# Kernel optimization log

Hardware: AMD Instinct MI355X
Metric: run time of the kernel (lower is better)

The kernel has to match this reference:

```python
import jax, jax.numpy as jnp
import numpy as np

B, N, D = 8, 4096, 2


def setup_inputs() -> dict:
    key = jax.random.key(0)
    k1, k2 = jax.random.split(key)
    y_true = jax.random.normal(k1, (B, N, D), dtype=jnp.float32)
    y_pred = jax.random.normal(k2, (B, N, D), dtype=jnp.float32)
    return {"y_true": y_true, "y_pred": y_pred}


def reference(y_true, y_pred):
    # Bidirectional Chamfer distance (chamferdist semantics):
    # squared-Euclidean NN distances, sum over points, mean over batch, both directions.
    xx = jnp.sum(y_true * y_true, axis=-1)                      # [B, N]
    yy = jnp.sum(y_pred * y_pred, axis=-1)                      # [B, N]
    xy = jnp.einsum('bnd,bmd->bnm', y_true, y_pred)             # [B, N, N]
    d2 = jnp.maximum(xx[:, :, None] + yy[:, None, :] - 2.0 * xy, 0.0)  # [B, N, N]
    cd_fwd = jnp.mean(jnp.sum(jnp.min(d2, axis=2), axis=1))     # true -> pred
    cd_bwd = jnp.mean(jnp.sum(jnp.min(d2, axis=1), axis=1))     # pred -> true
    # EMD approximation: cumsum over the last (coordinate) axis, squared diff, mean.
    emd = jnp.mean(jnp.mean(jnp.square(jnp.cumsum(y_true, axis=-1) - jnp.cumsum(y_pred, axis=-1)), axis=-1))
    return cd_fwd + cd_bwd + emd
```

## Files before the change

### kernel.cpp

```cpp
#include <hip/hip_runtime.h>
#include <math.h>

#define BB    8
#define NN    4096
#define DIRS  2
#define TPB   256
#define Q     16
#define RSIZE 128
#define RC    (NN / RSIZE)
#define CDN   (DIRS * BB * NN)
#define RBLK  128

__global__ __launch_bounds__(TPB) void chamfer_kernel(
    const float* __restrict__ y_true, const float* __restrict__ y_pred,
    float* __restrict__ part)
{
    __shared__ float4 refs[RSIZE];
    const int rc  = blockIdx.x;
    const int dir = blockIdx.y;
    const int b   = blockIdx.z;

    const float2* qbase = (const float2*)(dir == 0 ? y_true : y_pred) + (size_t)b * NN;
    const float2* rbase = (const float2*)(dir == 0 ? y_pred : y_true) + (size_t)b * NN;

    const int t = threadIdx.x;
    if (t < RSIZE) {
        float2 r = rbase[rc * RSIZE + t];
        refs[t] = make_float4(-2.f * r.x, -2.f * r.y,
                              r.x * r.x + r.y * r.y, 0.f);
    }
    __syncthreads();

    float qx[Q], qy[Q], m[Q];
    #pragma unroll
    for (int j = 0; j < Q; ++j) {
        float2 qv = qbase[j * TPB + t];
        qx[j] = qv.x; qy[j] = qv.y; m[j] = INFINITY;
    }

    #pragma unroll 4
    for (int k = 0; k < RSIZE; ++k) {
        float4 r = refs[k];
        #pragma unroll
        for (int j = 0; j < Q; ++j) {
            float d = fmaf(qy[j], r.y, fmaf(qx[j], r.x, r.z));
            m[j] = fminf(m[j], d);
        }
    }

    #pragma unroll
    for (int j = 0; j < Q; ++j) {
        int q = j * TPB + t;
        float v = fmaxf(m[j] + (qx[j] * qx[j] + qy[j] * qy[j]), 0.f);
        part[(size_t)rc * CDN + ((size_t)dir * BB + b) * NN + q] = v;
    }
}

__global__ __launch_bounds__(TPB) void reduce_kernel(
    const float* __restrict__ y_true, const float* __restrict__ y_pred,
    const float* __restrict__ part, float* __restrict__ blocksum)
{
    const float cd_scale  = 1.0f / (float)BB;
    const float emd_scale = 1.0f / (2.0f * (float)BB * (float)NN);

    float acc = 0.f;
    const int gsz = gridDim.x * blockDim.x;
    const int gid = blockIdx.x * blockDim.x + threadIdx.x;

    for (int i = gid; i < CDN; i += gsz) {
        float mv = part[i];
        #pragma unroll
        for (int rc = 1; rc < RC; ++rc)
            mv = fminf(mv, part[(size_t)rc * CDN + i]);
        acc += mv * cd_scale;
    }

    const float2* tp = (const float2*)y_true;
    const float2* pp = (const float2*)y_pred;
    for (int i = gid; i < BB * NN; i += gsz) {
        float2 tv = tp[i], pv = pp[i];
        float c1 = tv.x - pv.x;
        float c2 = (tv.x + tv.y) - (pv.x + pv.y);
        acc = fmaf(c1 * emd_scale, c1, acc);
        acc = fmaf(c2 * emd_scale, c2, acc);
    }

    #pragma unroll
    for (int off = 32; off > 0; off >>= 1)
        acc += __shfl_down(acc, off, 64);

    __shared__ float wsum[TPB / 64];
    const int lane = threadIdx.x & 63, wid = threadIdx.x >> 6;
    if (lane == 0) wsum[wid] = acc;
    __syncthreads();
    if (threadIdx.x == 0) {
        float s = 0.f;
        #pragma unroll
        for (int w = 0; w < TPB / 64; ++w) s += wsum[w];
        blocksum[blockIdx.x] = s;
    }
}

__global__ void final_kernel(const float* __restrict__ blocksum,
                             float* __restrict__ out)
{
    float v = blocksum[threadIdx.x] + blocksum[threadIdx.x + 64];
    #pragma unroll
    for (int off = 32; off > 0; off >>= 1)
        v += __shfl_down(v, off, 64);
    if (threadIdx.x == 0) out[0] = v;
}

extern "C" void kernel_launch(void* const* d_in, const int* in_sizes, int n_in,
                              void* d_out, int out_size, void* d_ws, size_t ws_size,
                              hipStream_t stream) {
    const float* y_true = (const float*)d_in[0];
    const float* y_pred = (const float*)d_in[1];
    float* out = (float*)d_out;

    float* part     = (float*)d_ws;
    float* blocksum = part + (size_t)RC * CDN;

    chamfer_kernel<<<dim3(RC, DIRS, BB), TPB, 0, stream>>>(y_true, y_pred, part);
    reduce_kernel<<<RBLK, TPB, 0, stream>>>(y_true, y_pred, part, blocksum);
    final_kernel<<<1, 64, 0, stream>>>(blocksum, out);
}
```

Measured before the change: 80.93 us.

## Fuse chamfer, reduce and final kernels into one cooperative kernel

Merges the three kernels into a single cooperative launch. A grid-wide sync separates the nearest-neighbour pass from the reduction, and each block then adds its partial sum to the output with an atomicAdd. Block 0 zeroes the output before the grid sync. This removes two kernel launches and the intermediate blocksum buffer, at the cost of a grid barrier, the cooperative-launch requirement that all 512 blocks be co-resident, and a float summation order that is no longer deterministic.

```diff
diff --git a/kernel.cpp b/kernel.cpp
--- a/kernel.cpp
+++ b/kernel.cpp
@@ -1,5 +1,8 @@
 #include <hip/hip_runtime.h>
+#include <hip/hip_cooperative_groups.h>
 #include <math.h>
+
+namespace cg = cooperative_groups;
 
 #define BB    8
 #define NN    4096
@@ -9,26 +12,31 @@
 #define RSIZE 128
 #define RC    (NN / RSIZE)
 #define CDN   (DIRS * BB * NN)
-#define RBLK  128
+#define NBLK  (RC * DIRS * BB)
 
-__global__ __launch_bounds__(TPB) void chamfer_kernel(
+__global__ __launch_bounds__(TPB) void fused_kernel(
     const float* __restrict__ y_true, const float* __restrict__ y_pred,
-    float* __restrict__ part)
+    float* __restrict__ part, float* __restrict__ out)
 {
     __shared__ float4 refs[RSIZE];
-    const int rc  = blockIdx.x;
-    const int dir = blockIdx.y;
-    const int b   = blockIdx.z;
+    __shared__ float wsum[TPB / 64];
+
+    const int bid = blockIdx.x;
+    const int rc  = bid & (RC - 1);
+    const int db  = bid >> 5;
+    const int dir = db >> 3;
+    const int b   = db & (BB - 1);
+    const int t   = threadIdx.x;
 
     const float2* qbase = (const float2*)(dir == 0 ? y_true : y_pred) + (size_t)b * NN;
     const float2* rbase = (const float2*)(dir == 0 ? y_pred : y_true) + (size_t)b * NN;
 
-    const int t = threadIdx.x;
     if (t < RSIZE) {
         float2 r = rbase[rc * RSIZE + t];
         refs[t] = make_float4(-2.f * r.x, -2.f * r.y,
                               r.x * r.x + r.y * r.y, 0.f);
     }
+    if (bid == 0 && t == 0) out[0] = 0.f;
     __syncthreads();
 
     float qx[Q], qy[Q], m[Q];
@@ -52,63 +60,48 @@
     for (int j = 0; j < Q; ++j) {
         int q = j * TPB + t;
         float v = fmaxf(m[j] + (qx[j] * qx[j] + qy[j] * qy[j]), 0.f);
-        part[(size_t)rc * CDN + ((size_t)dir * BB + b) * NN + q] = v;
+        part[(size_t)rc * CDN + (size_t)db * NN + q] = v;
     }
-}
 
-__global__ __launch_bounds__(TPB) void reduce_kernel(
-    const float* __restrict__ y_true, const float* __restrict__ y_pred,
-    const float* __restrict__ part, float* __restrict__ blocksum)
-{
+    cg::this_grid().sync();
+
     const float cd_scale  = 1.0f / (float)BB;
     const float emd_scale = 1.0f / (2.0f * (float)BB * (float)NN);
 
     float acc = 0.f;
-    const int gsz = gridDim.x * blockDim.x;
-    const int gid = blockIdx.x * blockDim.x + threadIdx.x;
 
-    for (int i = gid; i < CDN; i += gsz) {
+    if (t < 128) {
+        int i = bid * 128 + t;
         float mv = part[i];
         #pragma unroll
-        for (int rc = 1; rc < RC; ++rc)
-            mv = fminf(mv, part[(size_t)rc * CDN + i]);
+        for (int r = 1; r < RC; ++r)
+            mv = fminf(mv, part[(size_t)r * CDN + i]);
         acc += mv * cd_scale;
     }
 
-    const float2* tp = (const float2*)y_true;
-    const float2* pp = (const float2*)y_pred;
-    for (int i = gid; i < BB * NN; i += gsz) {
-        float2 tv = tp[i], pv = pp[i];
-        float c1 = tv.x - pv.x;
-        float c2 = (tv.x + tv.y) - (pv.x + pv.y);
-        acc = fmaf(c1 * emd_scale, c1, acc);
-        acc = fmaf(c2 * emd_scale, c2, acc);
+    {
+        int gid = bid * TPB + t;
+        if (gid < BB * NN) {
+            float2 tv = ((const float2*)y_true)[gid];
+            float2 pv = ((const float2*)y_pred)[gid];
+            float c1 = tv.x - pv.x;
+            float c2 = (tv.x + tv.y) - (pv.x + pv.y);
+            acc = fmaf(c1 * emd_scale, c1, acc);
+            acc = fmaf(c2 * emd_scale, c2, acc);
+        }
     }
 
     #pragma unroll
     for (int off = 32; off > 0; off >>= 1)
         acc += __shfl_down(acc, off, 64);
 
-    __shared__ float wsum[TPB / 64];
-    const int lane = threadIdx.x & 63, wid = threadIdx.x >> 6;
+    const int lane = t & 63, wid = t >> 6;
     if (lane == 0) wsum[wid] = acc;
     __syncthreads();
-    if (threadIdx.x == 0) {
-        float s = 0.f;
-        #pragma unroll
-        for (int w = 0; w < TPB / 64; ++w) s += wsum[w];
-        blocksum[blockIdx.x] = s;
+    if (t == 0) {
+        float s = wsum[0] + wsum[1] + wsum[2] + wsum[3];
+        atomicAdd(out, s);
     }
-}
-
-__global__ void final_kernel(const float* __restrict__ blocksum,
-                             float* __restrict__ out)
-{
-    float v = blocksum[threadIdx.x] + blocksum[threadIdx.x + 64];
-    #pragma unroll
-    for (int off = 32; off > 0; off >>= 1)
-        v += __shfl_down(v, off, 64);
-    if (threadIdx.x == 0) out[0] = v;
 }
 
 extern "C" void kernel_launch(void* const* d_in, const int* in_sizes, int n_in,
@@ -116,12 +109,10 @@
                               hipStream_t stream) {
     const float* y_true = (const float*)d_in[0];
     const float* y_pred = (const float*)d_in[1];
-    float* out = (float*)d_out;
+    float* out  = (float*)d_out;
+    float* part = (float*)d_ws;
 
-    float* part     = (float*)d_ws;
-    float* blocksum = part + (size_t)RC * CDN;
-
-    chamfer_kernel<<<dim3(RC, DIRS, BB), TPB, 0, stream>>>(y_true, y_pred, part);
-    reduce_kernel<<<RBLK, TPB, 0, stream>>>(y_true, y_pred, part, blocksum);
-    final_kernel<<<1, 64, 0, stream>>>(blocksum, out);
+    void* args[] = { (void*)&y_true, (void*)&y_pred, (void*)&part, (void*)&out };
+    hipLaunchCooperativeKernel((void*)fused_kernel, dim3(NBLK), dim3(TPB),
+                               args, 0, stream);
 }
```

Result: slower. 132.3 us (+63.5%).
